# Kernel optimization log

Measured on AMD Instinct MI355X. Metric: run time of the kernel, lower is better.

The kernel has to match this reference:

```python
import jax, jax.numpy as jnp
import numpy as np


def setup_inputs() -> dict:
    key = jax.random.key(0)
    B, R, A, T, S = 16, 1, 16, 14, 1024  # batch, num_rx, num_rx_ant, num_ofdm_symbols, num_eff_subcarriers
    k1, k2 = jax.random.split(key)
    y_real = jax.random.normal(k1, (B, R, A, T, S), dtype=jnp.float32)
    y_imag = jax.random.normal(k2, (B, R, A, T, S), dtype=jnp.float32)

    # Emulate PilotPattern-derived constants (computed in __init__ in the original):
    # zero-power pilot positions at OFDM symbols {2, 11}, every 2nd subcarrier.
    pilot_syms = np.array([2, 11], dtype=np.int64)
    est_sc = np.arange(0, S, 2, dtype=np.int64)  # estimated subcarriers (unique)
    sym_grid, sc_grid = np.meshgrid(pilot_syms, est_sc, indexing='ij')  # row-major like tf.where
    estimation_indices = jnp.asarray(
        np.stack([sym_grid.ravel(), sc_grid.ravel()], axis=1), dtype=jnp.int32)  # [P, 2]
    # Nearest estimated subcarrier for every subcarrier (np.argmin tie -> first, like original).
    closest = est_sc[np.argmin(np.abs(est_sc[None, :] - np.arange(S)[:, None]), axis=1)]
    closest_subcarrier = jnp.asarray(closest, dtype=jnp.int32)  # [S]

    return {"y_real": y_real, "y_imag": y_imag,
            "estimation_indices": estimation_indices,
            "closest_subcarrier": closest_subcarrier}


def reference(y_real, y_imag, estimation_indices, closest_subcarrier):
    y = jax.lax.complex(y_real, y_imag)  # [B,R,A,T,S] complex64
    B, R, A, T, S = y.shape
    sym = estimation_indices[:, 0]
    sc = estimation_indices[:, 1]

    # gather_nd over the (symbol, subcarrier) positions -> [B,R,A,P]
    sig = y[:, :, :, sym, sc]
    # per-position outer product over antennas -> [P,B,R,A,A]
    cov_el = jnp.einsum('brip,brjp->pbrij', sig, jnp.conj(sig))

    # unsorted_segment_mean over subcarrier ids (real/imag separately, as in TF)
    counts = jax.ops.segment_sum(jnp.ones_like(sc, dtype=jnp.float32), sc, num_segments=S)
    denom = jnp.maximum(counts, 1.0)[:, None, None, None, None]  # empty segments -> 0, like TF
    sum_r = jax.ops.segment_sum(cov_el.real, sc, num_segments=S)
    sum_i = jax.ops.segment_sum(cov_el.imag, sc, num_segments=S)
    cov_sw = jax.lax.complex(sum_r / denom, sum_i / denom)  # [S,B,R,A,A]

    # nearest-neighbor interpolation over subcarriers
    cov_nn = cov_sw[closest_subcarrier]                      # [S,B,R,A,A]
    cov = jnp.transpose(cov_nn, (1, 2, 0, 3, 4))             # [B,R,S,A,A]
    cov = cov[:, :, None]                                    # [B,R,1,S,A,A]
    return jnp.broadcast_to(cov, (B, R, T, S, A, A))
```

## Files before the change

kernel.cpp:

```cpp
#include <hip/hip_runtime.h>

static constexpr int kB = 16;
static constexpr int kA = 16;
static constexpr int kT = 14;
static constexpr int kS = 1024;
static constexpr int kMaxMatch = 32;

typedef __attribute__((ext_vector_type(4))) float fvec4;


static constexpr long kWsInts = 2048 + (long)kS * kMaxMatch;

__global__ __launch_bounds__(1024) void build_meta(
    const int* __restrict__ est,
    const int* __restrict__ closest,
    int*       __restrict__ wsi,
    int P)
{
    const int tid = threadIdx.x;

    bool est64 = true;
    {
        int lim = 2 * P; if (lim > 128) lim = 128;
        for (int k = 1; k < lim; k += 2)
            if (est[k] != 0) { est64 = false; break; }
    }
    bool clo64 = true;
    {
        int lim = kS; if (lim > 128) lim = 128;
        for (int k = 1; k < lim; k += 2)
            if (closest[k] != 0) { clo64 = false; break; }
    }

    if (tid < kS) {
        int c = closest[clo64 ? 2 * tid : tid];
        if (c < 0) c = 0;
        if (c >= kS) c = kS - 1;
        wsi[tid]        = c;
        wsi[kS + tid]   = 0;
    }
    __syncthreads();

    for (int p = tid; p < P; p += 1024) {
        const int sc = est[est64 ? 4 * p + 2 : 2 * p + 1];
        if (sc >= 0 && sc < kS) {
            const int sym = est[est64 ? 4 * p : 2 * p];
            if (sym >= 0 && sym < kT) {
                const int slot = atomicAdd(&wsi[kS + sc], 1);
                if (slot < kMaxMatch)
                    wsi[2 * kS + sc * kMaxMatch + slot] = sym;
            }
        }
    }
}

__global__ __launch_bounds__(256) void cov_linear(
    const float* __restrict__ y_real,
    const float* __restrict__ y_imag,
    const int*   __restrict__ wsi,
    fvec4*       __restrict__ out4,
    long out_floats)
{
    const int blk     = blockIdx.x;
    const int scChunk = blk & 31;
    const int bt      = blk >> 5;
    const int b       = bt / kT;
    const int s0      = scChunk * 32;
    const int tid     = threadIdx.x;

    __shared__ int   sm_c[32];
    __shared__ int   sm_cnt[32];
    __shared__ int   sm_sym[32][2];
    __shared__ float sm_re[32][kA];
    __shared__ float sm_im[32][kA];

    if (tid < 32) {
        const int c = wsi[s0 + tid];
        int cnt = wsi[kS + c];
        if (cnt > kMaxMatch) cnt = kMaxMatch;
        sm_c[tid]   = c;
        sm_cnt[tid] = cnt;
        sm_sym[tid][0] = (cnt > 0) ? wsi[2 * kS + c * kMaxMatch + 0] : 0;
        sm_sym[tid][1] = (cnt > 1) ? wsi[2 * kS + c * kMaxMatch + 1] : 0;
    }
    __syncthreads();

    int mmax = 0;
    #pragma unroll 8
    for (int r = 0; r < 32; ++r) {
        const int cr = sm_cnt[r];
        if (cr > mmax) mmax = cr;
    }

    fvec4 acc[16];
    #pragma unroll
    for (int k = 0; k < 16; ++k) acc[k] = (fvec4)0.f;

    const long bbase = (long)b * (kA * kT * kS);

    for (int m = 0; m < mmax; ++m) {
        #pragma unroll
        for (int k = 0; k < 4; ++k) {
            const int idx  = tid + 256 * k;
            const int half = idx >> 9;
            const int r    = (idx >> 4) & 31;
            const int a    = idx & 15;
            if (m < sm_cnt[r]) {
                const int sym = (m < 2) ? sm_sym[r][m]
                                        : wsi[2 * kS + sm_c[r] * kMaxMatch + m];
                const long off = bbase + (long)a * (kT * kS) + (long)sym * kS + sm_c[r];
                if (half == 0) sm_re[r][a] = y_real[off];
                else           sm_im[r][a] = y_imag[off];
            }
        }
        __syncthreads();

        #pragma unroll
        for (int k = 0; k < 16; ++k) {
            const int idx = tid + 256 * k;
            const int r   = idx >> 7;
            const int q   = idx & 127;
            if (m < sm_cnt[r]) {
                const int i  = q >> 3;
                const int j0 = (q & 7) * 2;
                const float xr  = sm_re[r][i],      xi  = sm_im[r][i];
                const float y0r = sm_re[r][j0],     y0i = sm_im[r][j0];
                const float y1r = sm_re[r][j0 + 1], y1i = sm_im[r][j0 + 1];
                acc[k].x += xr * y0r + xi * y0i;
                acc[k].y += xi * y0r - xr * y0i;
                acc[k].z += xr * y1r + xi * y1i;
                acc[k].w += xi * y1r - xr * y1i;
            }
        }
        __syncthreads();
    }

    const long base4 = (long)blk * 4096;
    if ((base4 + 4096) * 4 <= out_floats) {
        #pragma unroll
        for (int k = 0; k < 16; ++k) {
            const int idx = tid + 256 * k;
            const int r   = idx >> 7;
            const int cr  = sm_cnt[r];
            const float inv = 1.0f / (float)(cr > 0 ? cr : 1);
            fvec4 v = acc[k];
            v.x *= inv; v.y *= inv; v.z *= inv; v.w *= inv;
            __builtin_nontemporal_store(v, out4 + base4 + idx);
        }
    } else {
        #pragma unroll
        for (int k = 0; k < 16; ++k) {
            const int idx = tid + 256 * k;
            const int r   = idx >> 7;
            const int cr  = sm_cnt[r];
            const float inv = 1.0f / (float)(cr > 0 ? cr : 1);
            fvec4 v = acc[k];
            v.x *= inv; v.y *= inv; v.z *= inv; v.w *= inv;
            if ((base4 + idx + 1) * 4 <= out_floats)
                out4[base4 + idx] = v;
        }
    }
}

__global__ __launch_bounds__(64) void cov_real_kernel(
    const float* __restrict__ y_real,
    const float* __restrict__ y_imag,
    const int*   __restrict__ est,
    const int*   __restrict__ closest,
    float*       __restrict__ out,
    int P, long out_floats)
{
    const int blk = blockIdx.x;
    const int b   = blk >> 10;
    const int s   = blk & (kS - 1);
    const int tid = threadIdx.x;

    bool est64 = true;
    {
        int lim = 2 * P; if (lim > 128) lim = 128;
        for (int k = 1; k < lim; k += 2)
            if (est[k] != 0) { est64 = false; break; }
    }
    bool clo64 = true;
    {
        int lim = kS; if (lim > 128) lim = 128;
        for (int k = 1; k < lim; k += 2)
            if (closest[k] != 0) { clo64 = false; break; }
    }

    int c = closest[clo64 ? 2 * s : s];
    if (c < 0) c = 0;
    if (c >= kS) c = kS - 1;

    __shared__ int   sm_count;
    __shared__ int   sm_sym[kMaxMatch];
    __shared__ float sm_re[kA], sm_im[kA];

    if (tid == 0) sm_count = 0;
    __syncthreads();

    for (int p = tid; p < P; p += 64) {
        const int sc = est[est64 ? 4 * p + 2 : 2 * p + 1];
        if (sc == c) {
            const int sym = est[est64 ? 4 * p : 2 * p];
            if (sym >= 0 && sym < kT) {
                int slot = atomicAdd(&sm_count, 1);
                if (slot < kMaxMatch) sm_sym[slot] = sym;
            }
        }
    }
    __syncthreads();

    int count = sm_count;
    if (count > kMaxMatch) count = kMaxMatch;

    const int i  = tid >> 2;
    const int j0 = (tid & 3) * 4;

    float v0 = 0.f, v1 = 0.f, v2 = 0.f, v3 = 0.f;

    for (int m = 0; m < count; ++m) {
        const int sym = sm_sym[m];
        if (tid < kA) {
            const long off = (long)b * (kA * kT * kS) + (long)tid * (kT * kS)
                           + (long)sym * kS + c;
            sm_re[tid] = y_real[off];
            sm_im[tid] = y_imag[off];
        }
        __syncthreads();

        const float xr = sm_re[i], xi = sm_im[i];
        v0 += xr * sm_re[j0 + 0] + xi * sm_im[j0 + 0];
        v1 += xr * sm_re[j0 + 1] + xi * sm_im[j0 + 1];
        v2 += xr * sm_re[j0 + 2] + xi * sm_im[j0 + 2];
        v3 += xr * sm_re[j0 + 3] + xi * sm_im[j0 + 3];
        __syncthreads();
    }

    const float inv = 1.0f / (float)(count > 0 ? count : 1);
    const float4 v = make_float4(v0 * inv, v1 * inv, v2 * inv, v3 * inv);

    float4* __restrict__ out4 = (float4*)out;
    for (int t = 0; t < kT; ++t) {
        const long f4idx = ((long)(b * kT + t) * kS + s) * 64 + tid;
        if ((f4idx + 1) * 4 <= out_floats)
            out4[f4idx] = v;
    }
}

__global__ __launch_bounds__(128) void cov_cplx_kernel(
    const float* __restrict__ y_real,
    const float* __restrict__ y_imag,
    const int*   __restrict__ est,
    const int*   __restrict__ closest,
    float*       __restrict__ out,
    int P, long out_floats)
{
    const int blk = blockIdx.x;
    const int b   = blk >> 10;
    const int s   = blk & (kS - 1);
    const int tid = threadIdx.x;

    bool est64 = true;
    {
        int lim = 2 * P; if (lim > 128) lim = 128;
        for (int k = 1; k < lim; k += 2)
            if (est[k] != 0) { est64 = false; break; }
    }
    bool clo64 = true;
    {
        int lim = kS; if (lim > 128) lim = 128;
        for (int k = 1; k < lim; k += 2)
            if (closest[k] != 0) { clo64 = false; break; }
    }

    int c = closest[clo64 ? 2 * s : s];
    if (c < 0) c = 0;
    if (c >= kS) c = kS - 1;

    __shared__ int   sm_count;
    __shared__ int   sm_sym[kMaxMatch];
    __shared__ float sm_re[kA], sm_im[kA];

    if (tid == 0) sm_count = 0;
    __syncthreads();

    for (int p = tid; p < P; p += 128) {
        const int sc = est[est64 ? 4 * p + 2 : 2 * p + 1];
        if (sc == c) {
            const int sym = est[est64 ? 4 * p : 2 * p];
            if (sym >= 0 && sym < kT) {
                int slot = atomicAdd(&sm_count, 1);
                if (slot < kMaxMatch) sm_sym[slot] = sym;
            }
        }
    }
    __syncthreads();

    int count = sm_count;
    if (count > kMaxMatch) count = kMaxMatch;

    const int i  = tid >> 3;
    const int j0 = (tid & 7) * 2;

    float a0r = 0.f, a0i = 0.f, a1r = 0.f, a1i = 0.f;

    for (int m = 0; m < count; ++m) {
        const int sym = sm_sym[m];
        if (tid < kA) {
            const long off = (long)b * (kA * kT * kS) + (long)tid * (kT * kS)
                           + (long)sym * kS + c;
            sm_re[tid] = y_real[off];
            sm_im[tid] = y_imag[off];
        }
        __syncthreads();

        const float xr  = sm_re[i],      xi  = sm_im[i];
        const float y0r = sm_re[j0],     y0i = sm_im[j0];
        const float y1r = sm_re[j0 + 1], y1i = sm_im[j0 + 1];
        a0r += xr * y0r + xi * y0i;
        a0i += xi * y0r - xr * y0i;
        a1r += xr * y1r + xi * y1i;
        a1i += xi * y1r - xr * y1i;
        __syncthreads();
    }

    const float inv = 1.0f / (float)(count > 0 ? count : 1);
    const float4 v = make_float4(a0r * inv, a0i * inv, a1r * inv, a1i * inv);

    float4* __restrict__ out4 = (float4*)out;
    for (int t = 0; t < kT; ++t) {
        const long f4idx = ((long)(b * kT + t) * kS + s) * 128 + tid;
        if ((f4idx + 1) * 4 <= out_floats)
            out4[f4idx] = v;
    }
}

extern "C" void kernel_launch(void* const* d_in, const int* in_sizes, int n_in,
                              void* d_out, int out_size, void* d_ws, size_t ws_size,
                              hipStream_t stream) {
    const float* y_real  = (const float*)d_in[0];
    const float* y_imag  = (const float*)d_in[1];
    const int*   est     = (const int*)d_in[2];
    const int*   closest = (const int*)d_in[3];
    float*       out     = (float*)d_out;

    const int  P      = in_sizes[2] / 2;
    const long realN  = (long)kB * kT * kS * kA * kA;
    const long wsNeed = kWsInts * 4;

    if ((long)out_size >= 2 * realN) {
        if (ws_size >= (size_t)wsNeed) {
            int* wsi = (int*)d_ws;
            build_meta<<<dim3(1), dim3(1024), 0, stream>>>(est, closest, wsi, P);
            cov_linear<<<dim3(kB * kT * 32), dim3(256), 0, stream>>>(
                y_real, y_imag, wsi, (fvec4*)out, (long)out_size);
        } else {
            dim3 grid(kB * kS);
            cov_cplx_kernel<<<grid, dim3(128), 0, stream>>>(
                y_real, y_imag, est, closest, out, P, (long)out_size);
        }
    } else {
        dim3 grid(kB * kS);
        cov_real_kernel<<<grid, dim3(64), 0, stream>>>(
            y_real, y_imag, est, closest, out, P, (long)out_size);
    }
}
```

Measured before the change: 261.1 us.

## Compute covariance once per batch chunk and replicate stores across OFDM symbols

Result: no change. 262.7 us (+0.6%).

```diff
diff --git a/kernel.cpp b/kernel.cpp
--- a/kernel.cpp
+++ b/kernel.cpp
@@ -54,19 +54,17 @@
     }
 }
 
-__global__ __launch_bounds__(256) void cov_linear(
+__global__ __launch_bounds__(256) void cov_once(
     const float* __restrict__ y_real,
     const float* __restrict__ y_imag,
     const int*   __restrict__ wsi,
     fvec4*       __restrict__ out4,
     long out_floats)
 {
-    const int blk     = blockIdx.x;
-    const int scChunk = blk & 31;
-    const int bt      = blk >> 5;
-    const int b       = bt / kT;
-    const int s0      = scChunk * 32;
-    const int tid     = threadIdx.x;
+    const int b     = blockIdx.x >> 5;
+    const int chunk = blockIdx.x & 31;
+    const int s0    = chunk * 32;
+    const int tid   = threadIdx.x;
 
     __shared__ int   sm_c[32];
     __shared__ int   sm_cnt[32];
@@ -135,29 +133,33 @@
         __syncthreads();
     }
 
-    const long base4 = (long)blk * 4096;
-    if ((base4 + 4096) * 4 <= out_floats) {
-        #pragma unroll
-        for (int k = 0; k < 16; ++k) {
-            const int idx = tid + 256 * k;
-            const int r   = idx >> 7;
-            const int cr  = sm_cnt[r];
-            const float inv = 1.0f / (float)(cr > 0 ? cr : 1);
-            fvec4 v = acc[k];
-            v.x *= inv; v.y *= inv; v.z *= inv; v.w *= inv;
-            __builtin_nontemporal_store(v, out4 + base4 + idx);
+    #pragma unroll
+    for (int k = 0; k < 16; ++k) {
+        const int idx = tid + 256 * k;
+        const int cr  = sm_cnt[idx >> 7];
+        const float inv = 1.0f / (float)(cr > 0 ? cr : 1);
+        acc[k].x *= inv; acc[k].y *= inv; acc[k].z *= inv; acc[k].w *= inv;
+    }
+
+    const long lastBase = (long)((b * kT + (kT - 1)) * 32 + chunk) * 4096;
+    const bool fastAll  = (lastBase + 4096) * 4 <= out_floats;
+
+    if (fastAll) {
+        for (int t = 0; t < kT; ++t) {
+            const long base4 = (long)((b * kT + t) * 32 + chunk) * 4096;
+            #pragma unroll
+            for (int k = 0; k < 16; ++k)
+                __builtin_nontemporal_store(acc[k], out4 + base4 + tid + 256 * k);
         }
     } else {
-        #pragma unroll
-        for (int k = 0; k < 16; ++k) {
-            const int idx = tid + 256 * k;
-            const int r   = idx >> 7;
-            const int cr  = sm_cnt[r];
-            const float inv = 1.0f / (float)(cr > 0 ? cr : 1);
-            fvec4 v = acc[k];
-            v.x *= inv; v.y *= inv; v.z *= inv; v.w *= inv;
-            if ((base4 + idx + 1) * 4 <= out_floats)
-                out4[base4 + idx] = v;
+        for (int t = 0; t < kT; ++t) {
+            const long base4 = (long)((b * kT + t) * 32 + chunk) * 4096;
+            #pragma unroll
+            for (int k = 0; k < 16; ++k) {
+                const long idx4 = base4 + tid + 256 * k;
+                if ((idx4 + 1) * 4 <= out_floats)
+                    out4[idx4] = acc[k];
+            }
         }
     }
 }
@@ -353,7 +355,7 @@
         if (ws_size >= (size_t)wsNeed) {
             int* wsi = (int*)d_ws;
             build_meta<<<dim3(1), dim3(1024), 0, stream>>>(est, closest, wsi, P);
-            cov_linear<<<dim3(kB * kT * 32), dim3(256), 0, stream>>>(
+            cov_once<<<dim3(kB * 32), dim3(256), 0, stream>>>(
                 y_real, y_imag, wsi, (fvec4*)out, (long)out_size);
         } else {
             dim3 grid(kB * kS);
```
